# Kernel tuning notes

Measured on AMD Instinct MI355X. Metric: run time of the kernel, lower is better.

The kernel has to match this reference:

```python
import jax, jax.numpy as jnp
import numpy as np

N, E, IN, ED, H, HID, OUT, G = 50000, 800000, 128, 16, 4, 64, 128, 64
NEG_SLOPE = 0.2


def _glorot(key, shape):
    fan_in, fan_out = shape[0], shape[-1]
    lim = float(np.sqrt(6.0 / (fan_in + fan_out)))
    return jax.random.uniform(key, shape, jnp.float32, -lim, lim)


def setup_inputs() -> dict:
    key = jax.random.key(0)
    ks = jax.random.split(key, 32)
    inp = {}
    inp['x'] = jax.random.normal(ks[0], (N, IN), jnp.float32)
    inp['edge_index'] = jax.random.randint(ks[1], (2, E), 0, N)
    inp['edge_attr'] = jax.random.normal(ks[2], (E, ED), jnp.float32)
    inp['batch'] = jnp.sort(jax.random.randint(ks[3], (N,), 0, G))
    # layer dims: (in_channels, out_channels_per_head, concat)
    dims = [(IN, HID, True), (H * HID, HID, True), (H * HID, OUT, False)]
    k = 4
    for i, (cin, c, concat) in enumerate(dims):
        inp[f'W{i}'] = _glorot(ks[k], (cin, H * c)); k += 1
        inp[f'asrc{i}'] = _glorot(ks[k], (1, H, c)); k += 1
        inp[f'adst{i}'] = _glorot(ks[k], (1, H, c)); k += 1
        inp[f'We{i}'] = _glorot(ks[k], (ED, H * c)); k += 1
        inp[f'ae{i}'] = _glorot(ks[k], (1, H, c)); k += 1
        inp[f'b{i}'] = jnp.zeros((H * c if concat else c,), jnp.float32); k += 1
    return inp


def _gat_layer(x, src, dst, ea, W, asrc, adst, We, ae, b, c, concat):
    # PyG GATConv math (eval mode, shared lin for src/dst, edge_dim set).
    n = x.shape[0]
    h = (x @ W).reshape(n, H, c)                      # [N,H,C]
    a_s = (h * asrc).sum(-1)                          # [N,H]
    a_d = (h * adst).sum(-1)                          # [N,H]
    e = (ea @ We).reshape(-1, H, c)                   # [Etot,H,C]
    a_e = (e * ae).sum(-1)                            # [Etot,H]
    alpha = jax.nn.leaky_relu(a_s[src] + a_d[dst] + a_e, NEG_SLOPE)
    # numerically stable per-destination softmax (every dst has a self-loop)
    amax = jax.ops.segment_max(alpha, dst, num_segments=n)
    ex = jnp.exp(alpha - amax[dst])
    denom = jax.ops.segment_sum(ex, dst, num_segments=n)
    alpha = ex / (denom[dst] + 1e-16)
    out = jax.ops.segment_sum(h[src] * alpha[..., None], dst, num_segments=n)
    out = out.reshape(n, H * c) if concat else out.mean(axis=1)
    return out + b


def reference(x, edge_index, edge_attr, batch,
              W0, asrc0, adst0, We0, ae0, b0,
              W1, asrc1, adst1, We1, ae1, b1,
              W2, asrc2, adst2, We2, ae2, b2):
    n = x.shape[0]
    loop = jnp.arange(n)
    src = jnp.concatenate([edge_index[0], loop])
    dst = jnp.concatenate([edge_index[1], loop])
    # self-loop edge_attr uses fill_value='mean' (PyG default)
    ea = jnp.concatenate(
        [edge_attr, jnp.broadcast_to(edge_attr.mean(0), (n, edge_attr.shape[1]))], axis=0)
    h = _gat_layer(x, src, dst, ea, W0, asrc0, adst0, We0, ae0, b0, HID, True)
    h = jax.nn.elu(h)
    h = _gat_layer(h, src, dst, ea, W1, asrc1, adst1, We1, ae1, b1, HID, True)
    h = jax.nn.elu(h)
    h = _gat_layer(h, src, dst, ea, W2, asrc2, adst2, We2, ae2, b2, OUT, False)
    # global mean pool over graphs
    gsum = jax.ops.segment_sum(h, batch, num_segments=G)
    cnt = jax.ops.segment_sum(jnp.ones((n,), h.dtype), batch, num_segments=G)
    return gsum / jnp.maximum(cnt, 1.0)[:, None]
```

## Files before the change

### kernel.cpp

```cpp
#include <hip/hip_runtime.h>
#include <hip/hip_bf16.h>
#include <hip/hip_fp16.h>
#include <math.h>

#define N_NODES 50000
#define N_EDGES 800000
#define NHEADS  4
#define NEG_SLOPE 0.2f

typedef __attribute__((ext_vector_type(8))) _Float16 half8v;
typedef __attribute__((ext_vector_type(4))) float f32x4;

__device__ __forceinline__ void gld_lds16(const ushort* g, ushort* l) {
  __builtin_amdgcn_global_load_lds(
      (const __attribute__((address_space(1))) void*)g,
      (__attribute__((address_space(3))) void*)l, 16, 0, 0);
}

__device__ __forceinline__ void fma4(float4& a, uint2 r, float e) {
  __half2 p = *(__half2*)&r.x, q = *(__half2*)&r.y;
  float2 f = __half22float2(p), g2 = __half22float2(q);
  a.x += e * f.x; a.y += e * f.y; a.z += e * g2.x; a.w += e * g2.y;
}

__global__ void tofp16_kernel(const float* __restrict__ in, __half* __restrict__ out,
                              int n4) {
  int i = blockIdx.x * blockDim.x + threadIdx.x;
  if (i >= n4) return;
  float4 v = ((const float4*)in)[i];
  __half2 a = __floats2half2_rn(v.x, v.y);
  __half2 b = __floats2half2_rn(v.z, v.w);
  ((__half2*)out)[2 * i] = a;
  ((__half2*)out)[2 * i + 1] = b;
}

__global__ void splitT_all_kernel(const float* __restrict__ W0,
                                  const float* __restrict__ W1,
                                  const float* __restrict__ W2,
                                  __half* __restrict__ B0h, __half* __restrict__ B0l,
                                  __half* __restrict__ B1h, __half* __restrict__ B1l,
                                  __half* __restrict__ B2h, __half* __restrict__ B2l) {
  int i = blockIdx.x * 256 + threadIdx.x;
  if (i >= 229376) return;
  const float* W;
  __half *bh, *bl;
  int kshift, N, base;
  if (i < 32768)       { W = W0; bh = B0h; bl = B0l; kshift = 7; N = 256; base = 0; }
  else if (i < 98304)  { W = W1; bh = B1h; bl = B1l; kshift = 8; N = 256; base = 32768; }
  else                 { W = W2; bh = B2h; bl = B2l; kshift = 8; N = 512; base = 98304; }
  int j = i - base;
  int K = 1 << kshift;
  int nn = j >> kshift, k = j & (K - 1);
  float v = W[(size_t)k * N + nn];
  __half h = __float2half(v);
  bh[j] = h;
  bl[j] = __float2half(v - __half2float(h));
}

__global__ __launch_bounds__(256) void gemm_mfma_kernel(
    const __half* __restrict__ Ah, const __half* __restrict__ Bth,
    const __half* __restrict__ Btl, __half* __restrict__ h16,
    const float* __restrict__ asrc, const float* __restrict__ adst,
    float* __restrict__ a_s, float* __restrict__ a_d, int M, int K, int N, int Cph) {
  __shared__ ushort lds[3 * 4096];
  int tid = threadIdx.x;
  int lane = tid & 63, w = tid >> 6;
  int wm = w >> 1, wn = w & 1;
  int r16 = lane & 15, kgrp = lane >> 4;
  int bm = blockIdx.y * 128, bn = blockIdx.x * 128;

  const ushort* gp[6];
#pragma unroll
  for (int i = 0; i < 6; ++i) {
    int c = i * 256 + tid;
    int mmat = c >> 9;
    int s = c & 511;
    int row = s >> 2;
    int kg = (s & 3) ^ ((row >> 1) & 3);
    const ushort* base;
    int rowg;
    if (mmat == 0)      { base = (const ushort*)Ah;  rowg = min(bm + row, M - 1); }
    else if (mmat == 1) { base = (const ushort*)Bth; rowg = bn + row; }
    else                { base = (const ushort*)Btl; rowg = bn + row; }
    gp[i] = base + (size_t)rowg * K + kg * 8;
  }

  f32x4 acc[4][4] = {};
  for (int k0 = 0; k0 < K; k0 += 32) {
#pragma unroll
    for (int i = 0; i < 6; ++i)
      gld_lds16(gp[i] + k0, lds + i * 2048 + tid * 8);
    __syncthreads();
    half8v ah[4], bh[4], bl[4];
#pragma unroll
    for (int m = 0; m < 4; ++m) {
      int row = wm * 64 + m * 16 + r16;
      int s = row * 4 + (kgrp ^ ((row >> 1) & 3));
      ah[m] = *(const half8v*)(lds + 0 * 4096 + s * 8);
    }
#pragma unroll
    for (int j = 0; j < 4; ++j) {
      int row = wn * 64 + j * 16 + r16;
      int s = row * 4 + (kgrp ^ ((row >> 1) & 3));
      bh[j] = *(const half8v*)(lds + 1 * 4096 + s * 8);
      bl[j] = *(const half8v*)(lds + 2 * 4096 + s * 8);
    }
#pragma unroll
    for (int m = 0; m < 4; ++m)
#pragma unroll
      for (int j = 0; j < 4; ++j) {
        acc[m][j] = __builtin_amdgcn_mfma_f32_16x16x32_f16(ah[m], bh[j], acc[m][j], 0, 0, 0);
        acc[m][j] = __builtin_amdgcn_mfma_f32_16x16x32_f16(ah[m], bl[j], acc[m][j], 0, 0, 0);
      }
    __syncthreads();
  }

  int colbase = bn + wn * 64;
  int hd = colbase / Cph;
#pragma unroll
  for (int m = 0; m < 4; ++m) {
#pragma unroll
    for (int r = 0; r < 4; ++r) {
      int row = bm + wm * 64 + m * 16 + kgrp * 4 + r;
      bool ok = row < M;
      float ps = 0.f, pd = 0.f;
#pragma unroll
      for (int j = 0; j < 4; ++j) {
        float val = acc[m][j][r];
        int col = colbase + 16 * j + r16;
        if (ok) h16[(size_t)row * N + col] = __float2half(val);
        ps += val * asrc[col];
        pd += val * adst[col];
      }
#pragma unroll
      for (int o = 8; o >= 1; o >>= 1) {
        ps += __shfl_xor(ps, o);
        pd += __shfl_xor(pd, o);
      }
      if (r16 == 0 && ok) {
        atomicAdd(&a_s[row * NHEADS + hd], ps);
        atomicAdd(&a_d[row * NHEADS + hd], pd);
      }
    }
  }
}

__global__ void ea_colsum_kernel(const float* __restrict__ ea,
                                 float* __restrict__ sums, int E) {
  int tid = threadIdx.x;
  int col = tid & 15;
  float s = 0.f;
  for (int r = blockIdx.x * 16 + (tid >> 4); r < E; r += gridDim.x * 16)
    s += ea[(size_t)r * 16 + col];
  __shared__ float red[256];
  red[tid] = s;
  __syncthreads();
  for (int off = 128; off >= 16; off >>= 1) {
    if (tid < off) red[tid] += red[tid + off];
    __syncthreads();
  }
  if (tid < 16) atomicAdd(&sums[tid], red[tid]);
}

__global__ void wvec_kernel(const float* __restrict__ We0, const float* __restrict__ ae0,
                            const float* __restrict__ We1, const float* __restrict__ ae1,
                            const float* __restrict__ We2, const float* __restrict__ ae2,
                            const float* __restrict__ ea_sum,
                            float* __restrict__ wvec, float* __restrict__ ae_self) {
  __shared__ float sw[192];
  int tid = threadIdx.x;
  if (tid < 192) {
    int l = tid >> 6, rem = tid & 63, k = rem >> 2, hd = rem & 3;
    int C = (l == 2) ? 128 : 64;
    const float* We = (l == 0) ? We0 : (l == 1) ? We1 : We2;
    const float* ae = (l == 0) ? ae0 : (l == 1) ? ae1 : ae2;
    float s = 0.f;
    for (int c = 0; c < C; ++c) s += We[(size_t)k * (4 * C) + hd * C + c] * ae[hd * C + c];
    sw[tid] = s;
    wvec[tid] = s;
  }
  __syncthreads();
  if (tid < 12) {
    int l = tid >> 2, hd = tid & 3;
    const float invE = 1.0f / (float)N_EDGES;
    float s = 0.f;
    for (int k = 0; k < 16; ++k) s += ea_sum[k] * invE * sw[l * 64 + k * 4 + hd];
    ae_self[tid] = s;
  }
}

__global__ void deg_count_kernel(const int* __restrict__ dst, int* deg, int E) {
  int i = blockIdx.x * blockDim.x + threadIdx.x;
  int s = gridDim.x * blockDim.x;
  for (; i < E; i += s) atomicAdd(&deg[dst[i]], 1);
}

__global__ void scan_a_kernel(const int* __restrict__ deg, int* __restrict__ tmp,
                              int* __restrict__ bsum, int n) {
  __shared__ int s[256];
  int i = blockIdx.x * 256 + threadIdx.x;
  int v = (i < n) ? (deg[i] + 1) : 0;
  s[threadIdx.x] = v;
  __syncthreads();
  for (int d = 1; d < 256; d <<= 1) {
    int t = (threadIdx.x >= d) ? s[threadIdx.x - d] : 0;
    __syncthreads();
    s[threadIdx.x] += t;
    __syncthreads();
  }
  if (i < n) tmp[i] = s[threadIdx.x] - v;
  if (threadIdx.x == 255) bsum[blockIdx.x] = s[255];
}
__global__ void scan_b_kernel(int* bsum, int nb) {
  __shared__ int s[256];
  int v = (threadIdx.x < nb) ? bsum[threadIdx.x] : 0;
  s[threadIdx.x] = v;
  __syncthreads();
  for (int d = 1; d < 256; d <<= 1) {
    int t = (threadIdx.x >= d) ? s[threadIdx.x - d] : 0;
    __syncthreads();
    s[threadIdx.x] += t;
    __syncthreads();
  }
  if (threadIdx.x < nb) bsum[threadIdx.x] = s[threadIdx.x] - v;
}
__global__ void scan_c_kernel(const int* __restrict__ tmp, const int* __restrict__ bsum,
                              int* __restrict__ offsets, int* __restrict__ cursor,
                              int n, int tot) {
  int i = blockIdx.x * 256 + threadIdx.x;
  if (i < n) {
    int o = tmp[i] + bsum[blockIdx.x];
    offsets[i] = o;
    cursor[i] = o;
  }
  if (i == 0) offsets[n] = tot;
}

__global__ void scatter_kernel(const int* __restrict__ src, const int* __restrict__ dst,
                               int* cursor, uint2* __restrict__ csr_pack, int E, int n) {
  int i = blockIdx.x * blockDim.x + threadIdx.x;
  int s = gridDim.x * blockDim.x;
  int tot = E + n;
  for (; i < tot; i += s) {
    int ss, dd, eid;
    if (i < E) { ss = src[i]; dd = dst[i]; eid = i; }
    else       { ss = i - E; dd = ss;     eid = E; }
    int pos = atomicAdd(&cursor[dd], 1);
    csr_pack[pos] = make_uint2((uint)ss, (uint)eid);
  }
}

__global__ void ae_csr_kernel(const float* __restrict__ ea, const float* __restrict__ wv,
                              const float* __restrict__ ae_self,
                              const uint2* __restrict__ csr_pack,
                              float* __restrict__ aec, int* __restrict__ csr_src,
                              int tot, int E) {
  int i = blockIdx.x * blockDim.x + threadIdx.x;
  int stride = gridDim.x * blockDim.x;
  for (int p = i; p < tot; p += stride) {
    uint2 pk = csr_pack[p];
    int eid = (int)pk.y;
    csr_src[p] = (int)pk.x;
    if (eid >= E) {
#pragma unroll
      for (int l = 0; l < 3; ++l)
        *(float4*)(aec + ((size_t)l * tot + p) * 4) =
            make_float4(ae_self[l * 4 + 0], ae_self[l * 4 + 1],
                        ae_self[l * 4 + 2], ae_self[l * 4 + 3]);
    } else {
      float row[16];
      const float4* rp = (const float4*)(ea + (size_t)eid * 16);
#pragma unroll
      for (int q = 0; q < 4; ++q) {
        float4 v = rp[q];
        row[q * 4 + 0] = v.x; row[q * 4 + 1] = v.y;
        row[q * 4 + 2] = v.z; row[q * 4 + 3] = v.w;
      }
#pragma unroll
      for (int l = 0; l < 3; ++l) {
        float s0 = 0, s1 = 0, s2 = 0, s3 = 0;
#pragma unroll
        for (int k = 0; k < 16; ++k) {
          float v = row[k];
          s0 += v * wv[l * 64 + k * 4 + 0];
          s1 += v * wv[l * 64 + k * 4 + 1];
          s2 += v * wv[l * 64 + k * 4 + 2];
          s3 += v * wv[l * 64 + k * 4 + 3];
        }
        *(float4*)(aec + ((size_t)l * tot + p) * 4) = make_float4(s0, s1, s2, s3);
      }
    }
  }
}

template <int C, int MODE>
__global__ __launch_bounds__(256) void agg_kernel(
    const __half* __restrict__ h, const float* __restrict__ a_s,
    const float* __restrict__ a_d, const float* __restrict__ a_e,
    const int* __restrict__ offsets, const int* __restrict__ csr_src,
    const float* __restrict__ bias, __half* __restrict__ y16,
    float* __restrict__ yf) {
  constexpr int HC = NHEADS * C;
  constexpr int SL = HC / 4;
  constexpr int G = 256 / SL;
  constexpr int HSH = (C == 64) ? 4 : 5;

  __shared__ float exbuf[NHEADS][64];
  __shared__ int sbuf[64];
  __shared__ float dshare[NHEADS];
  __shared__ float4 cbuf4[(C == 64) ? 192 : 128];

  int node = blockIdx.x;
  int tid = threadIdx.x;
  int hd = tid >> 6, l = tid & 63;
  int beg = offsets[node], end = offsets[node + 1];
  int deg = end - beg;

  float a_dn = a_d[node * NHEADS + hd];

  int i = tid & (SL - 1);
  int g = tid / SL;
  int hh = i >> HSH;
  float4 acc = make_float4(0.f, 0.f, 0.f, 0.f);

  auto alpha_of = [&](int j, int& s_out) -> float {
    int s = csr_src[j];
    float aev = a_e[(size_t)j * NHEADS + hd];
    float v = a_s[s * NHEADS + hd] + a_dn + aev;
    s_out = s;
    return (v > 0.f) ? v : NEG_SLOPE * v;
  };

  auto accum_chunk = [&](int cnt) {
    int t = g;
    for (; t + 3 * G < cnt; t += 4 * G) {
      int s0 = sbuf[t], s1 = sbuf[t + G], s2 = sbuf[t + 2 * G], s3 = sbuf[t + 3 * G];
      float e0 = exbuf[hh][t], e1 = exbuf[hh][t + G];
      float e2 = exbuf[hh][t + 2 * G], e3 = exbuf[hh][t + 3 * G];
      uint2 r0 = *(const uint2*)(h + (size_t)s0 * HC + 4 * i);
      uint2 r1 = *(const uint2*)(h + (size_t)s1 * HC + 4 * i);
      uint2 r2 = *(const uint2*)(h + (size_t)s2 * HC + 4 * i);
      uint2 r3 = *(const uint2*)(h + (size_t)s3 * HC + 4 * i);
      fma4(acc, r0, e0); fma4(acc, r1, e1); fma4(acc, r2, e2); fma4(acc, r3, e3);
    }
    for (; t < cnt; t += G) {
      int s0 = sbuf[t];
      float e0 = exbuf[hh][t];
      uint2 r0 = *(const uint2*)(h + (size_t)s0 * HC + 4 * i);
      fma4(acc, r0, e0);
    }
  };

  if (deg <= 64) {
    int j = beg + l;
    bool valid = j < end;
    int s = 0;
    float al = -1e30f;
    if (valid) al = alpha_of(j, s);
    float m = al;
#pragma unroll
    for (int o = 32; o >= 1; o >>= 1) m = fmaxf(m, __shfl_xor(m, o));
    float ex = valid ? __expf(al - m) : 0.f;
    float dsum = ex;
#pragma unroll
    for (int o = 32; o >= 1; o >>= 1) dsum += __shfl_xor(dsum, o);
    exbuf[hd][l] = ex;
    if (hd == 0) sbuf[l] = s;
    if (l == 0) dshare[hd] = dsum;
    __syncthreads();
    accum_chunk(deg);
  } else {
    float m = -1e30f;
    for (int j0 = beg; j0 < end; j0 += 64) {
      int j = j0 + l;
      if (j < end) {
        int s;
        m = fmaxf(m, alpha_of(j, s));
      }
    }
#pragma unroll
    for (int o = 32; o >= 1; o >>= 1) m = fmaxf(m, __shfl_xor(m, o));
    float dsum = 0.f;
    for (int j0 = beg; j0 < end; j0 += 64) {
      int j = j0 + l;
      int cnt = min(64, end - j0);
      float ex = 0.f;
      int s = 0;
      if (j < end) {
        float al = alpha_of(j, s);
        ex = __expf(al - m);
      }
      dsum += ex;
      __syncthreads();
      exbuf[hd][l] = ex;
      if (hd == 0) sbuf[l] = s;
      __syncthreads();
      accum_chunk(cnt);
    }
#pragma unroll
    for (int o = 32; o >= 1; o >>= 1) dsum += __shfl_xor(dsum, o);
    if (l == 0) dshare[hd] = dsum;
    __syncthreads();
  }

  if (MODE == 0) {
    if (g > 0) cbuf4[(g - 1) * SL + i] = acc;
    __syncthreads();
    if (g == 0) {
      float4 c1 = cbuf4[i], c2 = cbuf4[SL + i], c3 = cbuf4[2 * SL + i];
      acc.x += c1.x + c2.x + c3.x;
      acc.y += c1.y + c2.y + c3.y;
      acc.z += c1.z + c2.z + c3.z;
      acc.w += c1.w + c2.w + c3.w;
      float inv = 1.f / (dshare[hh] + 1e-16f);
      const float4 bv = *(const float4*)(bias + 4 * i);
      float o0 = acc.x * inv + bv.x, o1 = acc.y * inv + bv.y;
      float o2 = acc.z * inv + bv.z, o3 = acc.w * inv + bv.w;
      o0 = (o0 > 0.f) ? o0 : (__expf(o0) - 1.f);
      o1 = (o1 > 0.f) ? o1 : (__expf(o1) - 1.f);
      o2 = (o2 > 0.f) ? o2 : (__expf(o2) - 1.f);
      o3 = (o3 > 0.f) ? o3 : (__expf(o3) - 1.f);
      __half2 w0 = __floats2half2_rn(o0, o1);
      __half2 w1 = __floats2half2_rn(o2, o3);
      uint2 pk;
      pk.x = *(uint*)&w0;
      pk.y = *(uint*)&w1;
      *(uint2*)(y16 + (size_t)node * HC + 4 * i) = pk;
    }
  } else {
    if (g == 1) cbuf4[i] = acc;
    __syncthreads();
    if (g == 0) {
      float4 c1 = cbuf4[i];
      float inv = 1.f / (dshare[hh] + 1e-16f);
      acc.x = (acc.x + c1.x) * inv;
      acc.y = (acc.y + c1.y) * inv;
      acc.z = (acc.z + c1.z) * inv;
      acc.w = (acc.w + c1.w) * inv;
    }
    __syncthreads();
    if (g == 0) cbuf4[i] = acc;
    __syncthreads();
    if (tid < 32) {
      float4 s0 = cbuf4[tid], s1 = cbuf4[tid + 32];
      float4 s2 = cbuf4[tid + 64], s3 = cbuf4[tid + 96];
      const float4 bv = *(const float4*)(bias + 4 * tid);
      float4 o;
      o.x = (s0.x + s1.x + s2.x + s3.x) * 0.25f + bv.x;
      o.y = (s0.y + s1.y + s2.y + s3.y) * 0.25f + bv.y;
      o.z = (s0.z + s1.z + s2.z + s3.z) * 0.25f + bv.z;
      o.w = (s0.w + s1.w + s2.w + s3.w) * 0.25f + bv.w;
      *(float4*)(yf + (size_t)node * 128 + 4 * tid) = o;
    }
  }
}

__global__ void pool_kernel(const float* __restrict__ y, const int* __restrict__ batch,
                            float* __restrict__ pool, float* __restrict__ cnt, int n) {
  int n0 = blockIdx.x * 256;
  if (n0 >= n) return;
  int n1 = min(n0 + 256, n);
  int c = threadIdx.x;
  float accum = 0.f;
  int cur = batch[n0];
  int cn = 0;
  for (int nd = n0; nd < n1; ++nd) {
    int g = batch[nd];
    if (g != cur) {
      atomicAdd(&pool[cur * 128 + c], accum);
      if (c == 0) atomicAdd(&cnt[cur], (float)cn);
      accum = 0.f; cn = 0; cur = g;
    }
    accum += y[(size_t)nd * 128 + c];
    cn++;
  }
  atomicAdd(&pool[cur * 128 + c], accum);
  if (c == 0) atomicAdd(&cnt[cur], (float)cn);
}
__global__ void finalize_kernel(const float* __restrict__ pool,
                                const float* __restrict__ cnt, float* __restrict__ out) {
  int i = blockIdx.x * blockDim.x + threadIdx.x;
  if (i < 64 * 128) out[i] = pool[i] / fmaxf(cnt[i >> 7], 1.f);
}

extern "C" void kernel_launch(void* const* d_in, const int* in_sizes, int n_in,
                              void* d_out, int out_size, void* d_ws, size_t ws_size,
                              hipStream_t stream) {
  const float* x = (const float*)d_in[0];
  const int* ei = (const int*)d_in[1];
  const float* ea = (const float*)d_in[2];
  const int* batch = (const int*)d_in[3];
  const float* W[3]    = {(const float*)d_in[4],  (const float*)d_in[10], (const float*)d_in[16]};
  const float* asrc[3] = {(const float*)d_in[5],  (const float*)d_in[11], (const float*)d_in[17]};
  const float* adst[3] = {(const float*)d_in[6],  (const float*)d_in[12], (const float*)d_in[18]};
  const float* Wep[3]  = {(const float*)d_in[7],  (const float*)d_in[13], (const float*)d_in[19]};
  const float* aep[3]  = {(const float*)d_in[8],  (const float*)d_in[14], (const float*)d_in[20]};
  const float* bp[3]   = {(const float*)d_in[9],  (const float*)d_in[15], (const float*)d_in[21]};

  char* ws = (char*)d_ws;
  size_t off = 0;
  auto take = [&](size_t bytes) -> void* {
    void* p = ws + off;
    off = (off + bytes + 255) & ~(size_t)255;
    return p;
  };
  const int TOT = N_EDGES + N_NODES;
  size_t zero_begin = off;
  float* ea_sum = (float*)take(16 * 4);
  float* pool   = (float*)take(8192 * 4);
  float* cnt    = (float*)take(64 * 4);
  int*   deg    = (int*)take((size_t)N_NODES * 4);
  float* a_sd   = (float*)take((size_t)3 * 2 * N_NODES * NHEADS * 4);
  size_t zero_bytes = off - zero_begin;

  float* wvec    = (float*)take(192 * 4);
  float* ae_self = (float*)take(12 * 4);
  int* tmp     = (int*)take((size_t)N_NODES * 4);
  int* bsum    = (int*)take(256 * 4);
  int* offsets = (int*)take(((size_t)N_NODES + 1) * 4);
  int* cursor  = (int*)take((size_t)N_NODES * 4);
  uint2* csr_pack = (uint2*)take((size_t)TOT * 8);
  int* csr_src = (int*)take((size_t)TOT * 4);
  float* aec  = (float*)take((size_t)3 * TOT * NHEADS * 4);
  __half* x16 = (__half*)take((size_t)N_NODES * 128 * 2);
  __half* Bh[3], *Bl[3];
  Bh[0] = (__half*)take((size_t)32768 * 2);  Bl[0] = (__half*)take((size_t)32768 * 2);
  Bh[1] = (__half*)take((size_t)65536 * 2);  Bl[1] = (__half*)take((size_t)65536 * 2);
  Bh[2] = (__half*)take((size_t)131072 * 2); Bl[2] = (__half*)take((size_t)131072 * 2);
  __half* h16 = (__half*)take((size_t)N_NODES * 512 * 2);
  __half* y16 = (__half*)take((size_t)N_NODES * 256 * 2);
  float* ybuf = (float*)take((size_t)N_NODES * 128 * 4);

  const int* srcp = ei;
  const int* dstp = ei + N_EDGES;
  const int NB = (N_NODES + 255) / 256;

  hipMemsetAsync(ws + zero_begin, 0, zero_bytes, stream);
  ea_colsum_kernel<<<512, 256, 0, stream>>>(ea, ea_sum, N_EDGES);
  deg_count_kernel<<<2048, 256, 0, stream>>>(dstp, deg, N_EDGES);
  scan_a_kernel<<<NB, 256, 0, stream>>>(deg, tmp, bsum, N_NODES);
  scan_b_kernel<<<1, 256, 0, stream>>>(bsum, NB);
  scan_c_kernel<<<NB, 256, 0, stream>>>(tmp, bsum, offsets, cursor, N_NODES, TOT);
  scatter_kernel<<<2048, 256, 0, stream>>>(srcp, dstp, cursor, csr_pack, N_EDGES, N_NODES);
  wvec_kernel<<<1, 256, 0, stream>>>(Wep[0], aep[0], Wep[1], aep[1], Wep[2], aep[2],
                                     ea_sum, wvec, ae_self);
  ae_csr_kernel<<<2048, 256, 0, stream>>>(ea, wvec, ae_self, csr_pack, aec, csr_src,
                                          TOT, N_EDGES);
  tofp16_kernel<<<(N_NODES * 128 / 4 + 255) / 256, 256, 0, stream>>>(x, x16,
                                                                     N_NODES * 128 / 4);
  splitT_all_kernel<<<(229376 + 255) / 256, 256, 0, stream>>>(
      W[0], W[1], W[2], Bh[0], Bl[0], Bh[1], Bl[1], Bh[2], Bl[2]);

  const __half* Acur = x16;
  for (int l = 0; l < 3; ++l) {
    int K = (l == 0) ? 128 : 256;
    int C = (l == 2) ? 128 : 64;
    int HC = NHEADS * C;
    float* a_s = a_sd + (size_t)l * 2 * N_NODES * NHEADS;
    float* a_d = a_s + (size_t)N_NODES * NHEADS;
    gemm_mfma_kernel<<<dim3(HC / 128, (N_NODES + 127) / 128), 256, 0, stream>>>(
        Acur, Bh[l], Bl[l], h16, asrc[l], adst[l], a_s, a_d, N_NODES, K, HC, C);
    if (l < 2) {
      agg_kernel<64, 0><<<N_NODES, 256, 0, stream>>>(
          h16, a_s, a_d, aec + (size_t)l * TOT * NHEADS, offsets, csr_src, bp[l],
          y16, nullptr);
      Acur = y16;
    } else {
      agg_kernel<128, 1><<<N_NODES, 256, 0, stream>>>(
          h16, a_s, a_d, aec + (size_t)l * TOT * NHEADS, offsets, csr_src, bp[l],
          nullptr, ybuf);
    }
  }
  pool_kernel<<<NB, 128, 0, stream>>>(ybuf, batch, pool, cnt, N_NODES);
  finalize_kernel<<<(8192 + 255) / 256, 256, 0, stream>>>(pool, cnt, (float*)d_out);
}
```

Measured before the change: 719.1 us.

## Restructure GAT aggregation to wave-per-head, four nodes per block, shuffle-based

The aggregation kernel changes from one node per block, which staged edge weights through shared memory with barriers, to four nodes per block. Each wave handles one head and keeps source ids and exp weights in registers, broadcasting them with shuffles. Each lane now loads one or two halves per edge instead of four, and the barriers and LDS cross-group reduction go away except for the final head mean in the last layer. Two pairs of small prep kernels (ea colsum with degree count, x cast with weight split) are also merged to cut launches. Narrower per-lane loads may reduce memory-level parallelism, and the grid assumes N is divisible by four.

Result: slower. 769.8 us (+7.0%).

```diff
diff --git a/kernel.cpp b/kernel.cpp
--- a/kernel.cpp
+++ b/kernel.cpp
@@ -17,44 +17,38 @@
       (__attribute__((address_space(3))) void*)l, 16, 0, 0);
 }
 
-__device__ __forceinline__ void fma4(float4& a, uint2 r, float e) {
-  __half2 p = *(__half2*)&r.x, q = *(__half2*)&r.y;
-  float2 f = __half22float2(p), g2 = __half22float2(q);
-  a.x += e * f.x; a.y += e * f.y; a.z += e * g2.x; a.w += e * g2.y;
-}
-
-__global__ void tofp16_kernel(const float* __restrict__ in, __half* __restrict__ out,
-                              int n4) {
-  int i = blockIdx.x * blockDim.x + threadIdx.x;
-  if (i >= n4) return;
-  float4 v = ((const float4*)in)[i];
-  __half2 a = __floats2half2_rn(v.x, v.y);
-  __half2 b = __floats2half2_rn(v.z, v.w);
-  ((__half2*)out)[2 * i] = a;
-  ((__half2*)out)[2 * i + 1] = b;
-}
-
-__global__ void splitT_all_kernel(const float* __restrict__ W0,
-                                  const float* __restrict__ W1,
-                                  const float* __restrict__ W2,
-                                  __half* __restrict__ B0h, __half* __restrict__ B0l,
-                                  __half* __restrict__ B1h, __half* __restrict__ B1l,
-                                  __half* __restrict__ B2h, __half* __restrict__ B2l) {
-  int i = blockIdx.x * 256 + threadIdx.x;
-  if (i >= 229376) return;
-  const float* W;
-  __half *bh, *bl;
-  int kshift, N, base;
-  if (i < 32768)       { W = W0; bh = B0h; bl = B0l; kshift = 7; N = 256; base = 0; }
-  else if (i < 98304)  { W = W1; bh = B1h; bl = B1l; kshift = 8; N = 256; base = 32768; }
-  else                 { W = W2; bh = B2h; bl = B2l; kshift = 8; N = 512; base = 98304; }
-  int j = i - base;
-  int K = 1 << kshift;
-  int nn = j >> kshift, k = j & (K - 1);
-  float v = W[(size_t)k * N + nn];
-  __half h = __float2half(v);
-  bh[j] = h;
-  bl[j] = __float2half(v - __half2float(h));
+__global__ void cast_all_kernel(const float* __restrict__ x, __half* __restrict__ x16,
+                                const float* __restrict__ W0,
+                                const float* __restrict__ W1,
+                                const float* __restrict__ W2,
+                                __half* __restrict__ B0h, __half* __restrict__ B0l,
+                                __half* __restrict__ B1h, __half* __restrict__ B1l,
+                                __half* __restrict__ B2h, __half* __restrict__ B2l) {
+  int b = blockIdx.x;
+  if (b < 6250) {
+    int i = b * 256 + threadIdx.x;
+    float4 v = ((const float4*)x)[i];
+    __half2 a = __floats2half2_rn(v.x, v.y);
+    __half2 c = __floats2half2_rn(v.z, v.w);
+    ((__half2*)x16)[2 * i] = a;
+    ((__half2*)x16)[2 * i + 1] = c;
+  } else {
+    int i = (b - 6250) * 256 + threadIdx.x;
+    if (i >= 229376) return;
+    const float* W;
+    __half *bh, *bl;
+    int kshift, N, base;
+    if (i < 32768)       { W = W0; bh = B0h; bl = B0l; kshift = 7; N = 256; base = 0; }
+    else if (i < 98304)  { W = W1; bh = B1h; bl = B1l; kshift = 8; N = 256; base = 32768; }
+    else                 { W = W2; bh = B2h; bl = B2l; kshift = 8; N = 512; base = 98304; }
+    int j = i - base;
+    int K = 1 << kshift;
+    int nn = j >> kshift, k = j & (K - 1);
+    float v = W[(size_t)k * N + nn];
+    __half h = __float2half(v);
+    bh[j] = h;
+    bl[j] = __float2half(v - __half2float(h));
+  }
 }
 
 __global__ __launch_bounds__(256) void gemm_mfma_kernel(
@@ -145,21 +139,27 @@
   }
 }
 
-__global__ void ea_colsum_kernel(const float* __restrict__ ea,
-                                 float* __restrict__ sums, int E) {
+__global__ void prep0_kernel(const float* __restrict__ ea, float* __restrict__ sums,
+                             const int* __restrict__ dst, int* __restrict__ deg, int E) {
   int tid = threadIdx.x;
-  int col = tid & 15;
-  float s = 0.f;
-  for (int r = blockIdx.x * 16 + (tid >> 4); r < E; r += gridDim.x * 16)
-    s += ea[(size_t)r * 16 + col];
-  __shared__ float red[256];
-  red[tid] = s;
-  __syncthreads();
-  for (int off = 128; off >= 16; off >>= 1) {
-    if (tid < off) red[tid] += red[tid + off];
-    __syncthreads();
-  }
-  if (tid < 16) atomicAdd(&sums[tid], red[tid]);
+  if (blockIdx.x < 512) {
+    int col = tid & 15;
+    float s = 0.f;
+    for (int r = blockIdx.x * 16 + (tid >> 4); r < E; r += 512 * 16)
+      s += ea[(size_t)r * 16 + col];
+    __shared__ float red[256];
+    red[tid] = s;
+    __syncthreads();
+    for (int off = 128; off >= 16; off >>= 1) {
+      if (tid < off) red[tid] += red[tid + off];
+      __syncthreads();
+    }
+    if (tid < 16) atomicAdd(&sums[tid], red[tid]);
+  } else {
+    int i = (blockIdx.x - 512) * 256 + tid;
+    int s = 2048 * 256;
+    for (; i < E; i += s) atomicAdd(&deg[dst[i]], 1);
+  }
 }
 
 __global__ void wvec_kernel(const float* __restrict__ We0, const float* __restrict__ ae0,
@@ -189,12 +189,6 @@
   }
 }
 
-__global__ void deg_count_kernel(const int* __restrict__ dst, int* deg, int E) {
-  int i = blockIdx.x * blockDim.x + threadIdx.x;
-  int s = gridDim.x * blockDim.x;
-  for (; i < E; i += s) atomicAdd(&deg[dst[i]], 1);
-}
-
 __global__ void scan_a_kernel(const int* __restrict__ deg, int* __restrict__ tmp,
                               int* __restrict__ bsum, int n) {
   __shared__ int s[256];
@@ -235,7 +229,6 @@
   }
   if (i == 0) offsets[n] = tot;
 }
-
 __global__ void scatter_kernel(const int* __restrict__ src, const int* __restrict__ dst,
                                int* cursor, uint2* __restrict__ csr_pack, int E, int n) {
   int i = blockIdx.x * blockDim.x + threadIdx.x;
@@ -293,165 +286,159 @@
   }
 }
 
-template <int C, int MODE>
-__global__ __launch_bounds__(256) void agg_kernel(
+template <int MODE>
+__global__ __launch_bounds__(256) void aggw_kernel(
     const __half* __restrict__ h, const float* __restrict__ a_s,
     const float* __restrict__ a_d, const float* __restrict__ a_e,
     const int* __restrict__ offsets, const int* __restrict__ csr_src,
     const float* __restrict__ bias, __half* __restrict__ y16,
     float* __restrict__ yf) {
-  constexpr int HC = NHEADS * C;
-  constexpr int SL = HC / 4;
-  constexpr int G = 256 / SL;
-  constexpr int HSH = (C == 64) ? 4 : 5;
-
-  __shared__ float exbuf[NHEADS][64];
-  __shared__ int sbuf[64];
-  __shared__ float dshare[NHEADS];
-  __shared__ float4 cbuf4[(C == 64) ? 192 : 128];
-
-  int node = blockIdx.x;
+  constexpr int NPB = 4;
   int tid = threadIdx.x;
-  int hd = tid >> 6, l = tid & 63;
-  int beg = offsets[node], end = offsets[node + 1];
-  int deg = end - beg;
-
-  float a_dn = a_d[node * NHEADS + hd];
-
-  int i = tid & (SL - 1);
-  int g = tid / SL;
-  int hh = i >> HSH;
-  float4 acc = make_float4(0.f, 0.f, 0.f, 0.f);
-
-  auto alpha_of = [&](int j, int& s_out) -> float {
-    int s = csr_src[j];
-    float aev = a_e[(size_t)j * NHEADS + hd];
-    float v = a_s[s * NHEADS + hd] + a_dn + aev;
-    s_out = s;
-    return (v > 0.f) ? v : NEG_SLOPE * v;
-  };
-
-  auto accum_chunk = [&](int cnt) {
-    int t = g;
-    for (; t + 3 * G < cnt; t += 4 * G) {
-      int s0 = sbuf[t], s1 = sbuf[t + G], s2 = sbuf[t + 2 * G], s3 = sbuf[t + 3 * G];
-      float e0 = exbuf[hh][t], e1 = exbuf[hh][t + G];
-      float e2 = exbuf[hh][t + 2 * G], e3 = exbuf[hh][t + 3 * G];
-      uint2 r0 = *(const uint2*)(h + (size_t)s0 * HC + 4 * i);
-      uint2 r1 = *(const uint2*)(h + (size_t)s1 * HC + 4 * i);
-      uint2 r2 = *(const uint2*)(h + (size_t)s2 * HC + 4 * i);
-      uint2 r3 = *(const uint2*)(h + (size_t)s3 * HC + 4 * i);
-      fma4(acc, r0, e0); fma4(acc, r1, e1); fma4(acc, r2, e2); fma4(acc, r3, e3);
-    }
-    for (; t < cnt; t += G) {
-      int s0 = sbuf[t];
-      float e0 = exbuf[hh][t];
-      uint2 r0 = *(const uint2*)(h + (size_t)s0 * HC + 4 * i);
-      fma4(acc, r0, e0);
-    }
-  };
-
-  if (deg <= 64) {
-    int j = beg + l;
-    bool valid = j < end;
+  int g = tid >> 6, l = tid & 63;
+  int nbase = blockIdx.x * NPB;
+
+  int beg[NPB], dg[NPB], sreg[NPB];
+  float exreg[NPB], inv[NPB], acc0[NPB], acc1[NPB];
+
+#pragma unroll
+  for (int it = 0; it < NPB; ++it) {
+    int nd = nbase + it;
+    int b0 = offsets[nd];
+    int d = offsets[nd + 1] - b0;
+    beg[it] = b0; dg[it] = d;
+    sreg[it] = 0; exreg[it] = 0.f; inv[it] = 0.f;
+    acc0[it] = 0.f; acc1[it] = 0.f;
+    if (d > 64) continue;
+    bool valid = l < d;
     int s = 0;
     float al = -1e30f;
-    if (valid) al = alpha_of(j, s);
+    if (valid) {
+      int j = b0 + l;
+      s = csr_src[j];
+      float aev = a_e[(size_t)j * NHEADS + g];
+      float v = a_s[s * NHEADS + g] + a_d[nd * NHEADS + g] + aev;
+      al = (v > 0.f) ? v : NEG_SLOPE * v;
+    }
     float m = al;
 #pragma unroll
     for (int o = 32; o >= 1; o >>= 1) m = fmaxf(m, __shfl_xor(m, o));
     float ex = valid ? __expf(al - m) : 0.f;
-    float dsum = ex;
-#pragma unroll
-    for (int o = 32; o >= 1; o >>= 1) dsum += __shfl_xor(dsum, o);
-    exbuf[hd][l] = ex;
-    if (hd == 0) sbuf[l] = s;
-    if (l == 0) dshare[hd] = dsum;
-    __syncthreads();
-    accum_chunk(deg);
-  } else {
+    float ds = ex;
+#pragma unroll
+    for (int o = 32; o >= 1; o >>= 1) ds += __shfl_xor(ds, o);
+    sreg[it] = s;
+    exreg[it] = ex;
+    inv[it] = 1.f / (ds + 1e-16f);
+  }
+
+#pragma unroll
+  for (int it = 0; it < NPB; ++it) {
+    int d = dg[it];
+    if (d > 64) continue;
+    int t = 0;
+    for (; t + 3 < d; t += 4) {
+      int st0 = __shfl(sreg[it], t),     st1 = __shfl(sreg[it], t + 1);
+      int st2 = __shfl(sreg[it], t + 2), st3 = __shfl(sreg[it], t + 3);
+      float e0 = __shfl(exreg[it], t),     e1 = __shfl(exreg[it], t + 1);
+      float e2 = __shfl(exreg[it], t + 2), e3 = __shfl(exreg[it], t + 3);
+      if (MODE == 0) {
+        float v0 = __half2float(h[(size_t)st0 * 256 + g * 64 + l]);
+        float v1 = __half2float(h[(size_t)st1 * 256 + g * 64 + l]);
+        float v2 = __half2float(h[(size_t)st2 * 256 + g * 64 + l]);
+        float v3 = __half2float(h[(size_t)st3 * 256 + g * 64 + l]);
+        acc0[it] += e0 * v0 + e1 * v1 + e2 * v2 + e3 * v3;
+      } else {
+        float2 f0 = __half22float2(*(const __half2*)(h + (size_t)st0 * 512 + g * 128 + 2 * l));
+        float2 f1 = __half22float2(*(const __half2*)(h + (size_t)st1 * 512 + g * 128 + 2 * l));
+        float2 f2 = __half22float2(*(const __half2*)(h + (size_t)st2 * 512 + g * 128 + 2 * l));
+        float2 f3 = __half22float2(*(const __half2*)(h + (size_t)st3 * 512 + g * 128 + 2 * l));
+        acc0[it] += e0 * f0.x + e1 * f1.x + e2 * f2.x + e3 * f3.x;
+        acc1[it] += e0 * f0.y + e1 * f1.y + e2 * f2.y + e3 * f3.y;
+      }
+    }
+    for (; t < d; ++t) {
+      int st = __shfl(sreg[it], t);
+      float e = __shfl(exreg[it], t);
+      if (MODE == 0) {
+        acc0[it] += e * __half2float(h[(size_t)st * 256 + g * 64 + l]);
+      } else {
+        float2 f = __half22float2(*(const __half2*)(h + (size_t)st * 512 + g * 128 + 2 * l));
+        acc0[it] += e * f.x;
+        acc1[it] += e * f.y;
+      }
+    }
+  }
+
+#pragma unroll
+  for (int it = 0; it < NPB; ++it) {
+    if (dg[it] <= 64) continue;
+    int nd = nbase + it;
+    int b0 = beg[it], end = b0 + dg[it];
+    float a_dn = a_d[nd * NHEADS + g];
     float m = -1e30f;
-    for (int j0 = beg; j0 < end; j0 += 64) {
+    for (int j0 = b0; j0 < end; j0 += 64) {
       int j = j0 + l;
       if (j < end) {
-        int s;
-        m = fmaxf(m, alpha_of(j, s));
+        int s = csr_src[j];
+        float v = a_s[s * NHEADS + g] + a_dn + a_e[(size_t)j * NHEADS + g];
+        float al = (v > 0.f) ? v : NEG_SLOPE * v;
+        m = fmaxf(m, al);
       }
     }
 #pragma unroll
     for (int o = 32; o >= 1; o >>= 1) m = fmaxf(m, __shfl_xor(m, o));
     float dsum = 0.f;
-    for (int j0 = beg; j0 < end; j0 += 64) {
+    for (int j0 = b0; j0 < end; j0 += 64) {
       int j = j0 + l;
       int cnt = min(64, end - j0);
+      int s = 0;
       float ex = 0.f;
-      int s = 0;
       if (j < end) {
-        float al = alpha_of(j, s);
+        s = csr_src[j];
+        float v = a_s[s * NHEADS + g] + a_dn + a_e[(size_t)j * NHEADS + g];
+        float al = (v > 0.f) ? v : NEG_SLOPE * v;
         ex = __expf(al - m);
       }
       dsum += ex;
-      __syncthreads();
-      exbuf[hd][l] = ex;
-      if (hd == 0) sbuf[l] = s;
-      __syncthreads();
-      accum_chunk(cnt);
+      for (int t = 0; t < cnt; ++t) {
+        int st = __shfl(s, t);
+        float e = __shfl(ex, t);
+        if (MODE == 0) {
+          acc0[it] += e * __half2float(h[(size_t)st * 256 + g * 64 + l]);
+        } else {
+          float2 f = __half22float2(*(const __half2*)(h + (size_t)st * 512 + g * 128 + 2 * l));
+          acc0[it] += e * f.x;
+          acc1[it] += e * f.y;
+        }
+      }
     }
 #pragma unroll
     for (int o = 32; o >= 1; o >>= 1) dsum += __shfl_xor(dsum, o);
-    if (l == 0) dshare[hd] = dsum;
-    __syncthreads();
+    inv[it] = 1.f / (dsum + 1e-16f);
   }
 
   if (MODE == 0) {
-    if (g > 0) cbuf4[(g - 1) * SL + i] = acc;
-    __syncthreads();
-    if (g == 0) {
-      float4 c1 = cbuf4[i], c2 = cbuf4[SL + i], c3 = cbuf4[2 * SL + i];
-      acc.x += c1.x + c2.x + c3.x;
-      acc.y += c1.y + c2.y + c3.y;
-      acc.z += c1.z + c2.z + c3.z;
-      acc.w += c1.w + c2.w + c3.w;
-      float inv = 1.f / (dshare[hh] + 1e-16f);
-      const float4 bv = *(const float4*)(bias + 4 * i);
-      float o0 = acc.x * inv + bv.x, o1 = acc.y * inv + bv.y;
-      float o2 = acc.z * inv + bv.z, o3 = acc.w * inv + bv.w;
-      o0 = (o0 > 0.f) ? o0 : (__expf(o0) - 1.f);
-      o1 = (o1 > 0.f) ? o1 : (__expf(o1) - 1.f);
-      o2 = (o2 > 0.f) ? o2 : (__expf(o2) - 1.f);
-      o3 = (o3 > 0.f) ? o3 : (__expf(o3) - 1.f);
-      __half2 w0 = __floats2half2_rn(o0, o1);
-      __half2 w1 = __floats2half2_rn(o2, o3);
-      uint2 pk;
-      pk.x = *(uint*)&w0;
-      pk.y = *(uint*)&w1;
-      *(uint2*)(y16 + (size_t)node * HC + 4 * i) = pk;
+    float bval = bias[g * 64 + l];
+#pragma unroll
+    for (int it = 0; it < NPB; ++it) {
+      int nd = nbase + it;
+      float o = acc0[it] * inv[it] + bval;
+      o = (o > 0.f) ? o : (__expf(o) - 1.f);
+      y16[(size_t)nd * 256 + g * 64 + l] = __float2half(o);
     }
   } else {
-    if (g == 1) cbuf4[i] = acc;
-    __syncthreads();
-    if (g == 0) {
-      float4 c1 = cbuf4[i];
-      float inv = 1.f / (dshare[hh] + 1e-16f);
-      acc.x = (acc.x + c1.x) * inv;
-      acc.y = (acc.y + c1.y) * inv;
-      acc.z = (acc.z + c1.z) * inv;
-      acc.w = (acc.w + c1.w) * inv;
-    }
-    __syncthreads();
-    if (g == 0) cbuf4[i] = acc;
-    __syncthreads();
-    if (tid < 32) {
-      float4 s0 = cbuf4[tid], s1 = cbuf4[tid + 32];
-      float4 s2 = cbuf4[tid + 64], s3 = cbuf4[tid + 96];
-      const float4 bv = *(const float4*)(bias + 4 * tid);
-      float4 o;
-      o.x = (s0.x + s1.x + s2.x + s3.x) * 0.25f + bv.x;
-      o.y = (s0.y + s1.y + s2.y + s3.y) * 0.25f + bv.y;
-      o.z = (s0.z + s1.z + s2.z + s3.z) * 0.25f + bv.z;
-      o.w = (s0.w + s1.w + s2.w + s3.w) * 0.25f + bv.w;
-      *(float4*)(yf + (size_t)node * 128 + 4 * tid) = o;
-    }
+    __shared__ float2 red[NPB][NHEADS][64];
+#pragma unroll
+    for (int it = 0; it < NPB; ++it)
+      red[it][g][l] = make_float2(acc0[it] * inv[it], acc1[it] * inv[it]);
+    __syncthreads();
+    int nd = nbase + g;
+    float2 s0 = red[g][0][l], s1 = red[g][1][l];
+    float2 s2 = red[g][2][l], s3 = red[g][3][l];
+    float o0 = (s0.x + s1.x + s2.x + s3.x) * 0.25f + bias[2 * l];
+    float o1 = (s0.y + s1.y + s2.y + s3.y) * 0.25f + bias[2 * l + 1];
+    *(float2*)(yf + (size_t)nd * 128 + 2 * l) = make_float2(o0, o1);
   }
 }
 
@@ -536,8 +523,7 @@
   const int NB = (N_NODES + 255) / 256;
 
   hipMemsetAsync(ws + zero_begin, 0, zero_bytes, stream);
-  ea_colsum_kernel<<<512, 256, 0, stream>>>(ea, ea_sum, N_EDGES);
-  deg_count_kernel<<<2048, 256, 0, stream>>>(dstp, deg, N_EDGES);
+  prep0_kernel<<<512 + 2048, 256, 0, stream>>>(ea, ea_sum, dstp, deg, N_EDGES);
   scan_a_kernel<<<NB, 256, 0, stream>>>(deg, tmp, bsum, N_NODES);
   scan_b_kernel<<<1, 256, 0, stream>>>(bsum, NB);
   scan_c_kernel<<<NB, 256, 0, stream>>>(tmp, bsum, offsets, cursor, N_NODES, TOT);
@@ -546,12 +532,11 @@
                                      ea_sum, wvec, ae_self);
   ae_csr_kernel<<<2048, 256, 0, stream>>>(ea, wvec, ae_self, csr_pack, aec, csr_src,
                                           TOT, N_EDGES);
-  tofp16_kernel<<<(N_NODES * 128 / 4 + 255) / 256, 256, 0, stream>>>(x, x16,
-                                                                     N_NODES * 128 / 4);
-  splitT_all_kernel<<<(229376 + 255) / 256, 256, 0, stream>>>(
-      W[0], W[1], W[2], Bh[0], Bl[0], Bh[1], Bl[1], Bh[2], Bl[2]);
+  cast_all_kernel<<<6250 + 896, 256, 0, stream>>>(x, x16, W[0], W[1], W[2], Bh[0], Bl[0],
+                                                  Bh[1], Bl[1], Bh[2], Bl[2]);
 
   const __half* Acur = x16;
+  const int AGGB = N_NODES / 4;
   for (int l = 0; l < 3; ++l) {
     int K = (l == 0) ? 128 : 256;
     int C = (l == 2) ? 128 : 64;
@@ -561,12 +546,12 @@
     gemm_mfma_kernel<<<dim3(HC / 128, (N_NODES + 127) / 128), 256, 0, stream>>>(
         Acur, Bh[l], Bl[l], h16, asrc[l], adst[l], a_s, a_d, N_NODES, K, HC, C);
     if (l < 2) {
-      agg_kernel<64, 0><<<N_NODES, 256, 0, stream>>>(
+      aggw_kernel<0><<<AGGB, 256, 0, stream>>>(
           h16, a_s, a_d, aec + (size_t)l * TOT * NHEADS, offsets, csr_src, bp[l],
           y16, nullptr);
       Acur = y16;
     } else {
-      agg_kernel<128, 1><<<N_NODES, 256, 0, stream>>>(
+      aggw_kernel<1><<<AGGB, 256, 0, stream>>>(
           h16, a_s, a_d, aec + (size_t)l * TOT * NHEADS, offsets, csr_src, bp[l],
           nullptr, ybuf);
     }
```
